# Kernel tuning notes

Hardware: AMD Instinct MI355X
Metric: run time of the kernel (lower is better)

Reference implementation:

```python
import jax, jax.numpy as jnp
import numpy as np

B = 32          # batch_size (scenes)
P_PER_B = 256   # proposals per scene (max_n_proposals, equal by construction)
N = B * P_PER_B # total proposals = 8192
PTS = 1024      # points per proposal
M = 128         # cfg.m, instance feature dim
LANG = 256      # lang_size
H = 128         # hidden_size
EPS = 1e-5      # BatchNorm eps


def setup_inputs() -> dict:
    key = jax.random.key(0)
    ks = jax.random.split(key, 16)
    feats = jax.random.normal(ks[0], (N, M), jnp.float32)
    total_pts = N * PTS
    # proposals_idx: (total_pts, 2) = [proposal_id, global_point_id]; points are
    # contiguous per proposal, proposals contiguous per scene.
    prop_ids = jnp.repeat(jnp.arange(N, dtype=jnp.int32), PTS)
    pt_ids = jnp.arange(total_pts, dtype=jnp.int32)
    proposals_idx = jnp.stack([prop_ids, pt_ids], axis=1)
    proposals_offset = jnp.arange(N + 1, dtype=jnp.int32) * PTS
    b_offsets = jnp.arange(B + 1, dtype=jnp.int32) * (P_PER_B * PTS)
    lang_emb = jax.random.normal(ks[1], (B, LANG), jnp.float32)
    # parameters: fuse = Conv1d(LANG+M -> H, k=1) + ReLU
    W_fuse = jax.random.normal(ks[2], (H, LANG + M), jnp.float32) * 0.05
    b_fuse = jnp.zeros((H,), jnp.float32)
    # match = Conv1d(H,H,1)+ReLU+BN, Conv1d(H,H,1)+ReLU+BN, Conv1d(H,1,1)
    W1 = jax.random.normal(ks[3], (H, H), jnp.float32) * 0.05
    b1 = jnp.zeros((H,), jnp.float32)
    g1 = jnp.ones((H,), jnp.float32)
    be1 = jnp.zeros((H,), jnp.float32)
    rm1 = jax.random.normal(ks[4], (H,), jnp.float32) * 0.1
    rv1 = jax.random.uniform(ks[5], (H,), jnp.float32, 0.5, 1.5)
    W2 = jax.random.normal(ks[6], (H, H), jnp.float32) * 0.05
    b2 = jnp.zeros((H,), jnp.float32)
    g2 = jnp.ones((H,), jnp.float32)
    be2 = jnp.zeros((H,), jnp.float32)
    rm2 = jax.random.normal(ks[7], (H,), jnp.float32) * 0.1
    rv2 = jax.random.uniform(ks[8], (H,), jnp.float32, 0.5, 1.5)
    W3 = jax.random.normal(ks[9], (1, H), jnp.float32) * 0.05
    b3 = jnp.zeros((1,), jnp.float32)
    return {
        'aggregated_vote_features': feats,
        'proposals_idx': proposals_idx,
        'proposals_offset': proposals_offset,
        'b_offsets': b_offsets,
        'lang_emb': lang_emb,
        'W_fuse': W_fuse, 'b_fuse': b_fuse,
        'W1': W1, 'b1': b1, 'g1': g1, 'be1': be1, 'rm1': rm1, 'rv1': rv1,
        'W2': W2, 'b2': b2, 'g2': g2, 'be2': be2, 'rm2': rm2, 'rv2': rv2,
        'W3': W3, 'b3': b3,
    }


def _bn(x, g, be, rm, rv):
    # eval-mode BatchNorm1d over channel dim of (B, C, P)
    scale = g / jnp.sqrt(rv + EPS)
    return (x - rm[None, :, None]) * scale[None, :, None] + be[None, :, None]


def reference(aggregated_vote_features, proposals_idx, proposals_offset, b_offsets,
              lang_emb, W_fuse, b_fuse, W1, b1, g1, be1, rm1, rv1,
              W2, b2, g2, be2, rm2, rv2, W3, b3):
    # --- vectorized replacement of the host-sync batch-id loop ---
    first_pts = proposals_idx[proposals_offset[:-1], 1]            # (N,) first point of each proposal
    bid = jnp.searchsorted(b_offsets, first_pts, side='right') - 1  # (N,) proposal_batch_ids
    # --- ragged -> padded gather (vectorized scatter by per-batch position) ---
    counts = jax.ops.segment_sum(jnp.ones_like(bid), bid, num_segments=B)
    offs = jnp.concatenate([jnp.zeros((1,), counts.dtype), jnp.cumsum(counts)[:-1]])
    order = jnp.argsort(bid)                                       # stable sort keeps original order per batch
    bid_s = bid[order]
    pos = jnp.arange(bid.shape[0]) - offs[bid_s]                   # position within its batch
    padded = jnp.zeros((B, P_PER_B, M), aggregated_vote_features.dtype)
    padded = padded.at[bid_s, pos].set(aggregated_vote_features[order])  # (B, P, M)
    # --- concat language features and run 1x1 conv chain ---
    lang = jnp.broadcast_to(lang_emb[:, None, :], (B, P_PER_B, LANG))
    x = jnp.concatenate([padded, lang], axis=-1)                   # (B, P, M+LANG)
    x = jnp.einsum('bpc,oc->bop', x, W_fuse) + b_fuse[None, :, None]
    x = jax.nn.relu(x)                                             # fuse
    x = _bn(jax.nn.relu(jnp.einsum('bcp,oc->bop', x, W1) + b1[None, :, None]), g1, be1, rm1, rv1)
    x = _bn(jax.nn.relu(jnp.einsum('bcp,oc->bop', x, W2) + b2[None, :, None]), g2, be2, rm2, rv2)
    conf = jnp.einsum('bcp,oc->bop', x, W3) + b3[None, :, None]    # (B, 1, P)
    return conf[:, 0, :]                                           # cluster_ref: (B, P)
```

## Files before the change

### kernel.cpp

```cpp
#include <hip/hip_runtime.h>
#include <math.h>

#define B_    32
#define PPB   256
#define N_    (B_*PPB)
#define M_    128
#define LANG_ 256
#define H_    128
#define EPS_  1e-5f
#define MC    32
#define NBLK  (N_/MC)

typedef __attribute__((ext_vector_type(8))) short s16x8;
typedef __attribute__((ext_vector_type(4))) float f32x4;
typedef unsigned long long ull_t;

static __device__ __forceinline__ unsigned short f2bf(float x) {
  unsigned int u = __float_as_uint(x);
  unsigned int r = (u + 0x7fff + ((u >> 16) & 1)) >> 16;
  return (unsigned short)r;
}
static __device__ __forceinline__ float bf2f(unsigned short h) {
  return __uint_as_float(((unsigned int)h) << 16);
}

__global__ __launch_bounds__(256) void k_prep(
    const int* __restrict__ pidx, const int* __restrict__ poff,
    int* __restrict__ fp_c,
    const float* __restrict__ Wf, const float* __restrict__ lang,
    float* __restrict__ lp,
    const float* __restrict__ W1, const float* __restrict__ W2,
    unsigned short* __restrict__ wa)
{
  const int tid = threadIdx.x;
  const int lane = tid & 63, wid = tid >> 6;
  const int o16 = lane & 15, g = lane >> 4;
  const int blk = blockIdx.x;

  if (blk < 32) {
    const int i = blk * 256 + tid;
    const int off = poff[i];
    __builtin_nontemporal_store(pidx[2 * off + 1], &fp_c[i]);
  } else if (blk < 64) {
    const int bb = blk - 32;
    const int o = tid >> 1, hf = tid & 1;
    float acc = 0.f;
    const int l0 = hf * 128;
    #pragma unroll 8
    for (int l = l0; l < l0 + 128; l += 4) {
      const float4 w = *reinterpret_cast<const float4*>(Wf + o * 384 + 128 + l);
      const float4 e = *reinterpret_cast<const float4*>(lang + bb * LANG_ + l);
      acc += w.x * e.x + w.y * e.y + w.z * e.z + w.w * e.w;
    }
    acc += __shfl_xor(acc, 1);
    if (hf == 0) __builtin_nontemporal_store(acc, &lp[bb * H_ + o]);
  } else {
    for (int sub = wid; sub < 6; sub += 4) {
      const int G = (blk - 64) * 6 + sub;
      const int L = G >> 6, s = (G >> 3) & 7, t = G & 7;
      const float* Wsrc; int str;
      if (L == 0)      { Wsrc = Wf; str = 384; }
      else if (L == 1) { Wsrc = W1; str = H_; }
      else             { Wsrc = W2; str = H_; }
      const int o = t * 16 + o16, sp = s & 3;
      const bool hi = (s < 4);
      const float* rowp = Wsrc + (size_t)o * str + sp * 32 + g * 4;
      const float4 a = *reinterpret_cast<const float4*>(rowp);
      const float4 bq = *reinterpret_cast<const float4*>(rowp + 16);
      const float av[8] = {a.x, a.y, a.z, a.w, bq.x, bq.y, bq.z, bq.w};
      union { s16x8 v; ull_t u[2]; } cv;
      #pragma unroll
      for (int e = 0; e < 8; ++e) {
        const unsigned short h = f2bf(av[e]);
        cv.v[e] = (short)(hi ? h : f2bf(av[e] - bf2f(h)));
      }
      ull_t* wp = reinterpret_cast<ull_t*>(wa + (size_t)G * 512 + lane * 8);
      __builtin_nontemporal_store(cv.u[0], wp);
      __builtin_nontemporal_store(cv.u[1], wp + 1);
    }
  }
}

#define LOAD_A(Aarr, LL)                                                     \
  {                                                                          \
    _Pragma("unroll")                                                        \
    for (int s = 0; s < 8; ++s)                                              \
      Aarr[s] = *reinterpret_cast<const s16x8*>(                             \
          wa + (size_t)(((LL) * 8 + s) * 8 + wid) * 512 + lane * 8);         \
  }

#define READ_B()                                                             \
  {                                                                          \
    _Pragma("unroll")                                                        \
    for (int s = 0; s < 4; ++s)                                              \
      _Pragma("unroll")                                                      \
      for (int nt = 0; nt < 2; ++nt) {                                       \
        const int idx = (s * 4 + g) * 32 + nt * 16 + o16;                    \
        Bh[s][nt] = XbHi[idx];                                               \
        Bl[s][nt] = XbLo[idx];                                               \
      }                                                                      \
  }

#define MFMA_LAYER(Aarr)                                                     \
  {                                                                          \
    _Pragma("unroll")                                                        \
    for (int sg = 0; sg < 8; ++sg)                                           \
      _Pragma("unroll")                                                      \
      for (int nt = 0; nt < 2; ++nt) {                                       \
        const s16x8 bb = (sg < 4) ? Bh[sg][nt] : Bl[sg - 4][nt];             \
        acc[nt] = __builtin_amdgcn_mfma_f32_16x16x32_bf16(Aarr[sg], bb, acc[nt], 0, 0, 0); \
      }                                                                      \
    _Pragma("unroll")                                                        \
    for (int sg = 0; sg < 8; ++sg)                                           \
      _Pragma("unroll")                                                      \
      for (int nt = 0; nt < 2; ++nt) {                                       \
        const s16x8 bb = (sg < 4) ? Bl[sg][nt] : Bh[sg - 4][nt];             \
        acc[nt] = __builtin_amdgcn_mfma_f32_16x16x32_bf16(Aarr[sg], bb, acc[nt], 0, 0, 0); \
      }                                                                      \
  }

#define ACT_STORE(EXPR_V)                                                    \
  {                                                                          \
    _Pragma("unroll")                                                        \
    for (int nt = 0; nt < 2; ++nt) {                                         \
      ull_t hv64 = 0, lv64 = 0;                                              \
      _Pragma("unroll")                                                      \
      for (int r = 0; r < 4; ++r) {                                          \
        const int o = wid * 16 + g * 4 + r;                                  \
        const float z = acc[nt][r];                                          \
        const float v = (EXPR_V);                                            \
        const unsigned short h = f2bf(v);                                    \
        const unsigned short l = f2bf(v - bf2f(h));                          \
        hv64 |= (ull_t)h << (16 * r);                                        \
        lv64 |= (ull_t)l << (16 * r);                                        \
      }                                                                      \
      const int f = ((wid >> 1) * 4 + g) * 32 + nt * 16 + o16;               \
      reinterpret_cast<ull_t*>(XbHi)[f * 2 + (wid & 1)] = hv64;              \
      reinterpret_cast<ull_t*>(XbLo)[f * 2 + (wid & 1)] = lv64;              \
    }                                                                        \
  }

__global__ __launch_bounds__(512, 2) void k_mlp(
    const float* __restrict__ feats,
    const unsigned short* __restrict__ wa,
    const int* __restrict__ fp_c, const int* __restrict__ boff,
    const float* __restrict__ bf, const float* __restrict__ b1,
    const float* __restrict__ g1, const float* __restrict__ be1,
    const float* __restrict__ rm1, const float* __restrict__ rv1,
    const float* __restrict__ b2, const float* __restrict__ g2,
    const float* __restrict__ be2, const float* __restrict__ rm2,
    const float* __restrict__ rv2,
    const float* __restrict__ W3, const float* __restrict__ b3,
    const float* __restrict__ lpg,
    float* __restrict__ out)
{
  __shared__ s16x8 XbHi[512];
  __shared__ s16x8 XbLo[512];
  __shared__ float pbuf[1024];
  __shared__ float outp[8][32];
  __shared__ int   sSrow[MC];
  __shared__ int   wtot[8];

  const int tid = threadIdx.x;
  const int lane = tid & 63, wid = tid >> 6;
  const int o16 = lane & 15, g = lane >> 4;
  const int q0 = blockIdx.x * MC;
  const int b = q0 >> 8;
  const int r0 = q0 & 255;

  if (tid < MC) sSrow[tid] = -1;
  const int blo = boff[b], bhi = boff[b + 1];
  const int i0 = tid * 16;
  unsigned mask = 0u;
  #pragma unroll
  for (int jj = 0; jj < 4; ++jj) {
    const int4 pv = *reinterpret_cast<const int4*>(fp_c + i0 + jj * 4);
    const int fps[4] = {pv.x, pv.y, pv.z, pv.w};
    #pragma unroll
    for (int e = 0; e < 4; ++e)
      mask |= (fps[e] >= blo && fps[e] < bhi) ? (1u << (jj * 4 + e)) : 0u;
  }
  const int cnt = __popc(mask);
  int sc = cnt;
  #pragma unroll
  for (int d = 1; d < 64; d <<= 1) {
    const int v = __shfl_up(sc, d);
    if (lane >= d) sc += v;
  }
  if (lane == 63) wtot[wid] = sc;
  __syncthreads();
  int base = sc - cnt;
  #pragma unroll
  for (int w = 0; w < 8; ++w) if (w < wid) base += wtot[w];
  {
    unsigned m = mask;
    int r = base;
    while (m) {
      const int j = __ffs(m) - 1;
      if (r >= r0 && r < r0 + MC) sSrow[r - r0] = i0 + j;
      ++r;
      m &= m - 1;
    }
  }

  s16x8 A0[8], A1[8], A2[8];
  LOAD_A(A0, 0);

  #pragma unroll
  for (int j = tid; j < 1024; j += 512) {
    const int arr = j >> 7, o = j & 127;
    float v;
    switch (arr) {
      case 0: v = bf[o] + lpg[b * H_ + o]; break;
      case 1: v = b1[o]; break;
      case 2: v = g1[o] * rsqrtf(rv1[o] + EPS_); break;
      case 3: { const float s = g1[o] * rsqrtf(rv1[o] + EPS_);
                v = be1[o] - rm1[o] * s; } break;
      case 4: v = b2[o]; break;
      case 5: v = g2[o] * rsqrtf(rv2[o] + EPS_); break;
      case 6: { const float s = g2[o] * rsqrtf(rv2[o] + EPS_);
                v = be2[o] - rm2[o] * s; } break;
      default: v = W3[o]; break;
    }
    pbuf[j] = v;
  }
  __syncthreads();

  {
    const int n = tid & 31, u = tid >> 5;
    const int s = u >> 2, gg = u & 3;
    const int srow = sSrow[n];
    const int k0 = s * 32 + gg * 4;
    float4 a = make_float4(0.f, 0.f, 0.f, 0.f), bq = a;
    if (srow >= 0) {
      a  = *reinterpret_cast<const float4*>(feats + (size_t)srow * M_ + k0);
      bq = *reinterpret_cast<const float4*>(feats + (size_t)srow * M_ + k0 + 16);
    }
    const float av[8] = {a.x, a.y, a.z, a.w, bq.x, bq.y, bq.z, bq.w};
    s16x8 hv, lv;
    #pragma unroll
    for (int e = 0; e < 8; ++e) {
      const unsigned short h = f2bf(av[e]);
      hv[e] = (short)h;
      lv[e] = (short)f2bf(av[e] - bf2f(h));
    }
    XbHi[u * 32 + n] = hv;
    XbLo[u * 32 + n] = lv;
  }
  __syncthreads();

  f32x4 acc[2];
  s16x8 Bh[4][2], Bl[4][2];

  READ_B();
  __syncthreads();
  LOAD_A(A1, 1);
  acc[0] = (f32x4){0.f, 0.f, 0.f, 0.f};
  acc[1] = (f32x4){0.f, 0.f, 0.f, 0.f};
  MFMA_LAYER(A0);
  ACT_STORE(fmaxf(z + pbuf[o], 0.f));
  __syncthreads();

  READ_B();
  __syncthreads();
  LOAD_A(A2, 2);
  acc[0] = (f32x4){0.f, 0.f, 0.f, 0.f};
  acc[1] = (f32x4){0.f, 0.f, 0.f, 0.f};
  MFMA_LAYER(A1);
  ACT_STORE(fmaxf(z + pbuf[128 + o], 0.f) * pbuf[256 + o] + pbuf[384 + o]);
  __syncthreads();

  READ_B();
  acc[0] = (f32x4){0.f, 0.f, 0.f, 0.f};
  acc[1] = (f32x4){0.f, 0.f, 0.f, 0.f};
  MFMA_LAYER(A2);
  {
    float p0 = 0.f, p1 = 0.f;
    #pragma unroll
    for (int r = 0; r < 4; ++r) {
      const int o = wid * 16 + g * 4 + r;
      const float w3 = pbuf[896 + o];
      const float bb2 = pbuf[512 + o], ss2 = pbuf[640 + o], tt2 = pbuf[768 + o];
      p0 += w3 * (fmaxf(acc[0][r] + bb2, 0.f) * ss2 + tt2);
      p1 += w3 * (fmaxf(acc[1][r] + bb2, 0.f) * ss2 + tt2);
    }
    p0 += __shfl_xor(p0, 16); p0 += __shfl_xor(p0, 32);
    p1 += __shfl_xor(p1, 16); p1 += __shfl_xor(p1, 32);
    if (lane < 16) {
      outp[wid][o16] = p0;
      outp[wid][16 + o16] = p1;
    }
    __syncthreads();
    if (tid < 32) {
      float s = b3[0];
      #pragma unroll
      for (int w = 0; w < 8; ++w) s += outp[w][tid];
      out[q0 + tid] = s;
    }
  }
}

extern "C" void kernel_launch(void* const* d_in, const int* in_sizes, int n_in,
                              void* d_out, int out_size, void* d_ws, size_t ws_size,
                              hipStream_t stream) {
  const float* feats = (const float*)d_in[0];
  const int*   pidx  = (const int*)d_in[1];
  const int*   poff  = (const int*)d_in[2];
  const int*   boff  = (const int*)d_in[3];
  const float* lang  = (const float*)d_in[4];
  const float* Wf    = (const float*)d_in[5];
  const float* bf    = (const float*)d_in[6];
  const float* W1    = (const float*)d_in[7];
  const float* b1    = (const float*)d_in[8];
  const float* g1    = (const float*)d_in[9];
  const float* be1   = (const float*)d_in[10];
  const float* rm1   = (const float*)d_in[11];
  const float* rv1   = (const float*)d_in[12];
  const float* W2    = (const float*)d_in[13];
  const float* b2    = (const float*)d_in[14];
  const float* g2    = (const float*)d_in[15];
  const float* be2   = (const float*)d_in[16];
  const float* rm2   = (const float*)d_in[17];
  const float* rv2   = (const float*)d_in[18];
  const float* W3    = (const float*)d_in[19];
  const float* b3    = (const float*)d_in[20];
  float* out = (float*)d_out;

  int*            fp_c = (int*)d_ws;
  float*          lp   = (float*)((char*)d_ws + 32768);
  unsigned short* wa   = (unsigned short*)((char*)d_ws + 49152);

  hipLaunchKernelGGL(k_prep, dim3(96), dim3(256), 0, stream,
                     pidx, poff, fp_c, Wf, lang, lp, W1, W2, wa);
  hipLaunchKernelGGL(k_mlp, dim3(NBLK), dim3(512), 0, stream,
                     feats, wa, fp_c, boff, bf, b1, g1, be1, rm1, rv1,
                     b2, g2, be2, rm2, rv2, W3, b3, lp, out);
}
```

Measured before the change: 20.54 us.

## Double-buffer activation LDS tiles and prefetch all layer weights upfront

The single shared-memory activation buffer is split into two ping-pong buffers, so each layer writes its output to the buffer the next layer reads from. This removes the barrier that sat between reading B fragments and storing the next activations. All three layers' weight fragments are also loaded into registers at kernel start, overlapping them with the index scan. The cost is double the LDS for activations and 192 extra live VGPRs held across the prologue, which may reduce occupancy under launch_bounds(512,2) or cause spills.

Result: slower. 22.11 us (median of 2 runs) (+7.7%).

```diff
diff --git a/kernel.cpp b/kernel.cpp
--- a/kernel.cpp
+++ b/kernel.cpp
@@ -89,15 +89,15 @@
           wa + (size_t)(((LL) * 8 + s) * 8 + wid) * 512 + lane * 8);         \
   }
 
-#define READ_B()                                                             \
+#define READ_B(SH, SL)                                                       \
   {                                                                          \
     _Pragma("unroll")                                                        \
     for (int s = 0; s < 4; ++s)                                              \
       _Pragma("unroll")                                                      \
       for (int nt = 0; nt < 2; ++nt) {                                       \
         const int idx = (s * 4 + g) * 32 + nt * 16 + o16;                    \
-        Bh[s][nt] = XbHi[idx];                                               \
-        Bl[s][nt] = XbLo[idx];                                               \
+        Bh[s][nt] = SH[idx];                                                 \
+        Bl[s][nt] = SL[idx];                                                 \
       }                                                                      \
   }
 
@@ -119,7 +119,7 @@
       }                                                                      \
   }
 
-#define ACT_STORE(EXPR_V)                                                    \
+#define ACT_STORE(SH, SL, EXPR_V)                                            \
   {                                                                          \
     _Pragma("unroll")                                                        \
     for (int nt = 0; nt < 2; ++nt) {                                         \
@@ -135,8 +135,8 @@
         lv64 |= (ull_t)l << (16 * r);                                        \
       }                                                                      \
       const int f = ((wid >> 1) * 4 + g) * 32 + nt * 16 + o16;               \
-      reinterpret_cast<ull_t*>(XbHi)[f * 2 + (wid & 1)] = hv64;              \
-      reinterpret_cast<ull_t*>(XbLo)[f * 2 + (wid & 1)] = lv64;              \
+      reinterpret_cast<ull_t*>(SH)[f * 2 + (wid & 1)] = hv64;                \
+      reinterpret_cast<ull_t*>(SL)[f * 2 + (wid & 1)] = lv64;                \
     }                                                                        \
   }
 
@@ -154,8 +154,8 @@
     const float* __restrict__ lpg,
     float* __restrict__ out)
 {
-  __shared__ s16x8 XbHi[512];
-  __shared__ s16x8 XbLo[512];
+  __shared__ s16x8 XbHiA[512], XbLoA[512];
+  __shared__ s16x8 XbHiB[512], XbLoB[512];
   __shared__ float pbuf[1024];
   __shared__ float outp[8][32];
   __shared__ int   sSrow[MC];
@@ -167,6 +167,11 @@
   const int q0 = blockIdx.x * MC;
   const int b = q0 >> 8;
   const int r0 = q0 & 255;
+
+  s16x8 A0[8], A1[8], A2[8];
+  LOAD_A(A0, 0);
+  LOAD_A(A1, 1);
+  LOAD_A(A2, 2);
 
   if (tid < MC) sSrow[tid] = -1;
   const int blo = boff[b], bhi = boff[b + 1];
@@ -202,9 +207,6 @@
       m &= m - 1;
     }
   }
-
-  s16x8 A0[8], A1[8], A2[8];
-  LOAD_A(A0, 0);
 
   #pragma unroll
   for (int j = tid; j < 1024; j += 512) {
@@ -244,33 +246,29 @@
       hv[e] = (short)h;
       lv[e] = (short)f2bf(av[e] - bf2f(h));
     }
-    XbHi[u * 32 + n] = hv;
-    XbLo[u * 32 + n] = lv;
+    XbHiA[u * 32 + n] = hv;
+    XbLoA[u * 32 + n] = lv;
   }
   __syncthreads();
 
   f32x4 acc[2];
   s16x8 Bh[4][2], Bl[4][2];
 
-  READ_B();
-  __syncthreads();
-  LOAD_A(A1, 1);
+  READ_B(XbHiA, XbLoA);
   acc[0] = (f32x4){0.f, 0.f, 0.f, 0.f};
   acc[1] = (f32x4){0.f, 0.f, 0.f, 0.f};
   MFMA_LAYER(A0);
-  ACT_STORE(fmaxf(z + pbuf[o], 0.f));
-  __syncthreads();
-
-  READ_B();
-  __syncthreads();
-  LOAD_A(A2, 2);
+  ACT_STORE(XbHiB, XbLoB, fmaxf(z + pbuf[o], 0.f));
+  __syncthreads();
+
+  READ_B(XbHiB, XbLoB);
   acc[0] = (f32x4){0.f, 0.f, 0.f, 0.f};
   acc[1] = (f32x4){0.f, 0.f, 0.f, 0.f};
   MFMA_LAYER(A1);
-  ACT_STORE(fmaxf(z + pbuf[128 + o], 0.f) * pbuf[256 + o] + pbuf[384 + o]);
-  __syncthreads();
-
-  READ_B();
+  ACT_STORE(XbHiA, XbLoA, fmaxf(z + pbuf[128 + o], 0.f) * pbuf[256 + o] + pbuf[384 + o]);
+  __syncthreads();
+
+  READ_B(XbHiA, XbLoA);
   acc[0] = (f32x4){0.f, 0.f, 0.f, 0.f};
   acc[1] = (f32x4){0.f, 0.f, 0.f, 0.f};
   MFMA_LAYER(A2);
```

## Split MLP block across 16 waves, one 16-column tile per wave

Applied to the files above, without the earlier changes.

Doubles the k_mlp block from 512 to 1024 threads. Each wave now handles one output-row tile and one 16-proposal column half, where before it handled both column halves. Per-wave MFMA work and register state are halved, which raises wave-level parallelism and lowers register pressure. In exchange, each weight A-fragment is loaded twice per block (once per column half), launch bounds drop the minimum-2-blocks hint, and the final reduction is reindexed across 16 waves.

New measurement: 20.99 us, median of 2. 1.02x slower.

```diff
diff --git a/kernel.cpp b/kernel.cpp
--- a/kernel.cpp
+++ b/kernel.cpp
@@ -86,61 +86,52 @@
     _Pragma("unroll")                                                        \
     for (int s = 0; s < 8; ++s)                                              \
       Aarr[s] = *reinterpret_cast<const s16x8*>(                             \
-          wa + (size_t)(((LL) * 8 + s) * 8 + wid) * 512 + lane * 8);         \
+          wa + (size_t)(((LL) * 8 + s) * 8 + ot) * 512 + lane * 8);          \
   }
 
 #define READ_B()                                                             \
   {                                                                          \
     _Pragma("unroll")                                                        \
-    for (int s = 0; s < 4; ++s)                                              \
-      _Pragma("unroll")                                                      \
-      for (int nt = 0; nt < 2; ++nt) {                                       \
-        const int idx = (s * 4 + g) * 32 + nt * 16 + o16;                    \
-        Bh[s][nt] = XbHi[idx];                                               \
-        Bl[s][nt] = XbLo[idx];                                               \
-      }                                                                      \
+    for (int s = 0; s < 4; ++s) {                                            \
+      const int idx = (s * 4 + g) * 32 + nth * 16 + o16;                     \
+      Bh[s] = XbHi[idx];                                                     \
+      Bl[s] = XbLo[idx];                                                     \
+    }                                                                        \
   }
 
 #define MFMA_LAYER(Aarr)                                                     \
   {                                                                          \
     _Pragma("unroll")                                                        \
-    for (int sg = 0; sg < 8; ++sg)                                           \
-      _Pragma("unroll")                                                      \
-      for (int nt = 0; nt < 2; ++nt) {                                       \
-        const s16x8 bb = (sg < 4) ? Bh[sg][nt] : Bl[sg - 4][nt];             \
-        acc[nt] = __builtin_amdgcn_mfma_f32_16x16x32_bf16(Aarr[sg], bb, acc[nt], 0, 0, 0); \
-      }                                                                      \
-    _Pragma("unroll")                                                        \
-    for (int sg = 0; sg < 8; ++sg)                                           \
-      _Pragma("unroll")                                                      \
-      for (int nt = 0; nt < 2; ++nt) {                                       \
-        const s16x8 bb = (sg < 4) ? Bl[sg][nt] : Bh[sg - 4][nt];             \
-        acc[nt] = __builtin_amdgcn_mfma_f32_16x16x32_bf16(Aarr[sg], bb, acc[nt], 0, 0, 0); \
-      }                                                                      \
+    for (int sg = 0; sg < 8; ++sg) {                                         \
+      const s16x8 bb = (sg < 4) ? Bh[sg] : Bl[sg - 4];                       \
+      acc = __builtin_amdgcn_mfma_f32_16x16x32_bf16(Aarr[sg], bb, acc, 0, 0, 0); \
+    }                                                                        \
+    _Pragma("unroll")                                                        \
+    for (int sg = 0; sg < 8; ++sg) {                                         \
+      const s16x8 bb = (sg < 4) ? Bl[sg] : Bh[sg - 4];                       \
+      acc = __builtin_amdgcn_mfma_f32_16x16x32_bf16(Aarr[sg], bb, acc, 0, 0, 0); \
+    }                                                                        \
   }
 
 #define ACT_STORE(EXPR_V)                                                    \
   {                                                                          \
-    _Pragma("unroll")                                                        \
-    for (int nt = 0; nt < 2; ++nt) {                                         \
-      ull_t hv64 = 0, lv64 = 0;                                              \
-      _Pragma("unroll")                                                      \
-      for (int r = 0; r < 4; ++r) {                                          \
-        const int o = wid * 16 + g * 4 + r;                                  \
-        const float z = acc[nt][r];                                          \
-        const float v = (EXPR_V);                                            \
-        const unsigned short h = f2bf(v);                                    \
-        const unsigned short l = f2bf(v - bf2f(h));                          \
-        hv64 |= (ull_t)h << (16 * r);                                        \
-        lv64 |= (ull_t)l << (16 * r);                                        \
-      }                                                                      \
-      const int f = ((wid >> 1) * 4 + g) * 32 + nt * 16 + o16;               \
-      reinterpret_cast<ull_t*>(XbHi)[f * 2 + (wid & 1)] = hv64;              \
-      reinterpret_cast<ull_t*>(XbLo)[f * 2 + (wid & 1)] = lv64;              \
+    ull_t hv64 = 0, lv64 = 0;                                                \
+    _Pragma("unroll")                                                        \
+    for (int r = 0; r < 4; ++r) {                                            \
+      const int o = ot * 16 + g * 4 + r;                                     \
+      const float z = acc[r];                                                \
+      const float v = (EXPR_V);                                              \
+      const unsigned short h = f2bf(v);                                      \
+      const unsigned short l = f2bf(v - bf2f(h));                            \
+      hv64 |= (ull_t)h << (16 * r);                                          \
+      lv64 |= (ull_t)l << (16 * r);                                          \
     }                                                                        \
-  }
-
-__global__ __launch_bounds__(512, 2) void k_mlp(
+    const int f = ((ot >> 1) * 4 + g) * 32 + nth * 16 + o16;                 \
+    reinterpret_cast<ull_t*>(XbHi)[f * 2 + (ot & 1)] = hv64;                 \
+    reinterpret_cast<ull_t*>(XbLo)[f * 2 + (ot & 1)] = lv64;                 \
+  }
+
+__global__ __launch_bounds__(1024) void k_mlp(
     const float* __restrict__ feats,
     const unsigned short* __restrict__ wa,
     const int* __restrict__ fp_c, const int* __restrict__ boff,
@@ -157,12 +148,13 @@
   __shared__ s16x8 XbHi[512];
   __shared__ s16x8 XbLo[512];
   __shared__ float pbuf[1024];
-  __shared__ float outp[8][32];
+  __shared__ float outp[16][16];
   __shared__ int   sSrow[MC];
-  __shared__ int   wtot[8];
+  __shared__ int   wtot[16];
 
   const int tid = threadIdx.x;
-  const int lane = tid & 63, wid = tid >> 6;
+  const int lane = tid & 63, w = tid >> 6;
+  const int ot = w & 7, nth = w >> 3;
   const int o16 = lane & 15, g = lane >> 4;
   const int q0 = blockIdx.x * MC;
   const int b = q0 >> 8;
@@ -170,10 +162,10 @@
 
   if (tid < MC) sSrow[tid] = -1;
   const int blo = boff[b], bhi = boff[b + 1];
-  const int i0 = tid * 16;
+  const int i0 = tid * 8;
   unsigned mask = 0u;
   #pragma unroll
-  for (int jj = 0; jj < 4; ++jj) {
+  for (int jj = 0; jj < 2; ++jj) {
     const int4 pv = *reinterpret_cast<const int4*>(fp_c + i0 + jj * 4);
     const int fps[4] = {pv.x, pv.y, pv.z, pv.w};
     #pragma unroll
@@ -187,11 +179,11 @@
     const int v = __shfl_up(sc, d);
     if (lane >= d) sc += v;
   }
-  if (lane == 63) wtot[wid] = sc;
+  if (lane == 63) wtot[w] = sc;
   __syncthreads();
   int base = sc - cnt;
   #pragma unroll
-  for (int w = 0; w < 8; ++w) if (w < wid) base += wtot[w];
+  for (int w2 = 0; w2 < 16; ++w2) if (w2 < w) base += wtot[w2];
   {
     unsigned m = mask;
     int r = base;
@@ -206,9 +198,8 @@
   s16x8 A0[8], A1[8], A2[8];
   LOAD_A(A0, 0);
 
-  #pragma unroll
-  for (int j = tid; j < 1024; j += 512) {
-    const int arr = j >> 7, o = j & 127;
+  {
+    const int arr = tid >> 7, o = tid & 127;
     float v;
     switch (arr) {
       case 0: v = bf[o] + lpg[b * H_ + o]; break;
@@ -222,11 +213,11 @@
                 v = be2[o] - rm2[o] * s; } break;
       default: v = W3[o]; break;
     }
-    pbuf[j] = v;
-  }
-  __syncthreads();
-
-  {
+    pbuf[tid] = v;
+  }
+  __syncthreads();
+
+  if (tid < 512) {
     const int n = tid & 31, u = tid >> 5;
     const int s = u >> 2, gg = u & 3;
     const int srow = sSrow[n];
@@ -249,14 +240,13 @@
   }
   __syncthreads();
 
-  f32x4 acc[2];
-  s16x8 Bh[4][2], Bl[4][2];
+  f32x4 acc;
+  s16x8 Bh[4], Bl[4];
 
   READ_B();
   __syncthreads();
   LOAD_A(A1, 1);
-  acc[0] = (f32x4){0.f, 0.f, 0.f, 0.f};
-  acc[1] = (f32x4){0.f, 0.f, 0.f, 0.f};
+  acc = (f32x4){0.f, 0.f, 0.f, 0.f};
   MFMA_LAYER(A0);
   ACT_STORE(fmaxf(z + pbuf[o], 0.f));
   __syncthreads();
@@ -264,37 +254,31 @@
   READ_B();
   __syncthreads();
   LOAD_A(A2, 2);
-  acc[0] = (f32x4){0.f, 0.f, 0.f, 0.f};
-  acc[1] = (f32x4){0.f, 0.f, 0.f, 0.f};
+  acc = (f32x4){0.f, 0.f, 0.f, 0.f};
   MFMA_LAYER(A1);
   ACT_STORE(fmaxf(z + pbuf[128 + o], 0.f) * pbuf[256 + o] + pbuf[384 + o]);
   __syncthreads();
 
   READ_B();
-  acc[0] = (f32x4){0.f, 0.f, 0.f, 0.f};
-  acc[1] = (f32x4){0.f, 0.f, 0.f, 0.f};
+  acc = (f32x4){0.f, 0.f, 0.f, 0.f};
   MFMA_LAYER(A2);
   {
-    float p0 = 0.f, p1 = 0.f;
+    float p0 = 0.f;
     #pragma unroll
     for (int r = 0; r < 4; ++r) {
-      const int o = wid * 16 + g * 4 + r;
-      const float w3 = pbuf[896 + o];
-      const float bb2 = pbuf[512 + o], ss2 = pbuf[640 + o], tt2 = pbuf[768 + o];
-      p0 += w3 * (fmaxf(acc[0][r] + bb2, 0.f) * ss2 + tt2);
-      p1 += w3 * (fmaxf(acc[1][r] + bb2, 0.f) * ss2 + tt2);
-    }
-    p0 += __shfl_xor(p0, 16); p0 += __shfl_xor(p0, 32);
-    p1 += __shfl_xor(p1, 16); p1 += __shfl_xor(p1, 32);
-    if (lane < 16) {
-      outp[wid][o16] = p0;
-      outp[wid][16 + o16] = p1;
-    }
+      const int o = ot * 16 + g * 4 + r;
+      p0 += pbuf[896 + o] *
+            (fmaxf(acc[r] + pbuf[512 + o], 0.f) * pbuf[640 + o] + pbuf[768 + o]);
+    }
+    p0 += __shfl_xor(p0, 16);
+    p0 += __shfl_xor(p0, 32);
+    if (lane < 16) outp[w][o16] = p0;
     __syncthreads();
     if (tid < 32) {
+      const int nt2 = tid >> 4, c16 = tid & 15;
       float s = b3[0];
       #pragma unroll
-      for (int w = 0; w < 8; ++w) s += outp[w][tid];
+      for (int o2 = 0; o2 < 8; ++o2) s += outp[nt2 * 8 + o2][c16];
       out[q0 + tid] = s;
     }
   }
@@ -332,7 +316,7 @@
 
   hipLaunchKernelGGL(k_prep, dim3(96), dim3(256), 0, stream,
                      pidx, poff, fp_c, Wf, lang, lp, W1, W2, wa);
-  hipLaunchKernelGGL(k_mlp, dim3(NBLK), dim3(512), 0, stream,
+  hipLaunchKernelGGL(k_mlp, dim3(NBLK), dim3(1024), 0, stream,
                      feats, wa, fp_c, boff, bf, b1, g1, be1, rm1, rv1,
                      b2, g2, be2, rm2, rv2, W3, b3, lp, out);
 }
```
